# Optimization experiments

Measured on AMD Instinct MI355X. Metric: run time of the kernel, lower is better.

## Reference

```python
import jax, jax.numpy as jnp
import numpy as np

B, N, K = 4, 2048, 30
H = 128   # num_hidden == num_V_dim
E = 128   # num_E_dim
SCALE = 30.0
EPS = 1e-5


def _ln(x, g, b):
    m = jnp.mean(x, axis=-1, keepdims=True)
    v = jnp.mean(jnp.square(x - m), axis=-1, keepdims=True)
    return (x - m) * jax.lax.rsqrt(v + EPS) * g + b


def _gather_nodes(h_V, E_idx):
    # h_V: [B,N,D], E_idx: [B,N,K] -> [B,N,K,D]
    b, n, k = E_idx.shape
    flat = E_idx.reshape(b, n * k)
    g = jnp.take_along_axis(h_V, flat[:, :, None], axis=1)
    return g.reshape(b, n, k, h_V.shape[-1])


def _gelu(x):
    return jax.nn.gelu(x, approximate=False)  # torch GELU default (erf)


def _lin(x, w, b):
    return jnp.einsum('...i,oi->...o', x, w) + b


def setup_inputs() -> dict:
    key = jax.random.key(0)
    ks = jax.random.split(key, 24)
    s = 0.05
    inp = {
        'h_V': jax.random.normal(ks[0], (B, N, H), jnp.float32),
        'h_E': jax.random.normal(ks[1], (B, N, K, E), jnp.float32),
        'E_idx': jax.random.randint(ks[2], (B, N, K), 0, N, jnp.int32),
        'mask_V': jnp.ones((B, N), jnp.float32),
        'mask_attend': jnp.ones((B, N, K), jnp.float32),
        # node-update MLP W1,W2,W3
        'W1_w': jax.random.normal(ks[3], (H, E + 2 * H), jnp.float32) * s,
        'W1_b': jnp.zeros((H,), jnp.float32),
        'W2_w': jax.random.normal(ks[4], (H, H), jnp.float32) * s,
        'W2_b': jnp.zeros((H,), jnp.float32),
        'W3_w': jax.random.normal(ks[5], (H, H), jnp.float32) * s,
        'W3_b': jnp.zeros((H,), jnp.float32),
        # edge-update MLP W11,W12,W13
        'W11_w': jax.random.normal(ks[6], (H, E + 2 * H), jnp.float32) * s,
        'W11_b': jnp.zeros((H,), jnp.float32),
        'W12_w': jax.random.normal(ks[7], (H, H), jnp.float32) * s,
        'W12_b': jnp.zeros((H,), jnp.float32),
        'W13_w': jax.random.normal(ks[8], (E, H), jnp.float32) * s,
        'W13_b': jnp.zeros((E,), jnp.float32),
        # dense FFN
        'Win_w': jax.random.normal(ks[9], (4 * H, H), jnp.float32) * s,
        'Win_b': jnp.zeros((4 * H,), jnp.float32),
        'Wout_w': jax.random.normal(ks[10], (H, 4 * H), jnp.float32) * s,
        'Wout_b': jnp.zeros((H,), jnp.float32),
        # layer norms
        'g1': jnp.ones((H,), jnp.float32), 'b1': jnp.zeros((H,), jnp.float32),
        'g2': jnp.ones((H,), jnp.float32), 'b2': jnp.zeros((H,), jnp.float32),
        'g3': jnp.ones((E,), jnp.float32), 'b3': jnp.zeros((E,), jnp.float32),
    }
    return inp


def reference(h_V, h_E, E_idx, mask_V, mask_attend,
              W1_w, W1_b, W2_w, W2_b, W3_w, W3_b,
              W11_w, W11_b, W12_w, W12_b, W13_w, W13_b,
              Win_w, Win_b, Wout_w, Wout_b,
              g1, b1, g2, b2, g3, b3):
    # --- node update ---
    nb = _gather_nodes(h_V, E_idx)                               # [B,N,K,H]
    hV_exp = jnp.broadcast_to(h_V[:, :, None, :], nb.shape)
    h_EV = jnp.concatenate([hV_exp, h_E, nb], axis=-1)           # [B,N,K,E+2H]
    m = _lin(_gelu(_lin(_gelu(_lin(h_EV, W1_w, W1_b)), W2_w, W2_b)), W3_w, W3_b)
    m = mask_attend[..., None] * m
    dh = jnp.sum(m, axis=-2) / SCALE
    h_V = _ln(h_V + dh, g1, b1)
    dh = _lin(_gelu(_lin(h_V, Win_w, Win_b)), Wout_w, Wout_b)
    h_V = _ln(h_V + dh, g2, b2)
    h_V = mask_V[..., None] * h_V
    # --- edge update ---
    nb = _gather_nodes(h_V, E_idx)
    hV_exp = jnp.broadcast_to(h_V[:, :, None, :], nb.shape)
    h_EV = jnp.concatenate([hV_exp, h_E, nb], axis=-1)
    m = _lin(_gelu(_lin(_gelu(_lin(h_EV, W11_w, W11_b)), W12_w, W12_b)), W13_w, W13_b)
    h_E = _ln(h_E + m, g3, b3)
    return h_V, h_E
```

## Files before the change

kernel.cpp:

```cpp
#include <hip/hip_runtime.h>
#include <math.h>

#define Kn    30
#define Hn    128
#define NB    2048
#define YS    136

#define OFF_W1    0
#define OFF_W2    49152
#define OFF_W3    65536
#define OFF_W11   81920
#define OFF_W12   131072
#define OFF_W13   147456
#define OFF_WIN   163840
#define OFF_WOUT  229376
#define W_TOTAL   294912
#define WS_ZM     524288
#define WS_SS     1048576
#define WS_SN     2097152

typedef __attribute__((ext_vector_type(8)))  short bh8;
typedef __attribute__((ext_vector_type(4)))  short bh4;
typedef __attribute__((ext_vector_type(16))) float fx16;

__device__ __forceinline__ unsigned short f2bf(float f) {
    unsigned int u = __float_as_uint(f);
    u += 0x7fffu + ((u >> 16) & 1u);
    return (unsigned short)(u >> 16);
}
__device__ __forceinline__ float bf2f(unsigned short h) {
    return __uint_as_float(((unsigned int)h) << 16);
}
__device__ __forceinline__ float gelu_f(float x) {
    float x2 = x * x;
    float p  = fmaf(x2, -0.10294415f, -2.30218409f);
    float e  = exp2f(x * p);
    return x * __builtin_amdgcn_rcpf(1.0f + e);
}
__device__ __forceinline__ fx16 mfma_bf16(bh8 a, bh8 b, fx16 c) {
    return __builtin_amdgcn_mfma_f32_32x32x16_bf16(a, b, c, 0, 0, 0);
}
__device__ __forceinline__ void st_bf4(unsigned short* dst, float4 v) {
    bh4 t;
    t.x = (short)f2bf(v.x); t.y = (short)f2bf(v.y);
    t.z = (short)f2bf(v.z); t.w = (short)f2bf(v.w);
    *(bh4*)dst = t;
}

template<int KS>
__device__ __forceinline__ void gemm_one(const unsigned short* __restrict__ aBase,
                                         const unsigned short* __restrict__ b0,
                                         fx16& acc0) {
    #pragma unroll
    for (int ks = 0; ks < KS; ks++) {
        bh8 a = *(const bh8*)(aBase + ks * 16);
        acc0 = mfma_bf16(a, *(const bh8*)(b0 + ks * 16), acc0);
    }
}

__device__ __forceinline__ void epi1_gelu_sg(const fx16& ac, int col,
                                             float bias, const float* __restrict__ sSelf,
                                             const float* __restrict__ nbrCol,
                                             const int* __restrict__ sIdx,
                                             unsigned short* __restrict__ dst, int lane) {
    int ro = 4 * (lane >> 5);
    float st = sSelf[col] + bias;
    #pragma unroll
    for (int r = 0; r < 16; r++) {
        int row = ro + (r & 3) + 8 * (r >> 2);
        float pn = nbrCol[(size_t)sIdx[row] * Hn];
        dst[row * YS + col] = f2bf(gelu_f(ac[r] + st + pn));
    }
}
__device__ __forceinline__ void epi1_gelu(const fx16& ac, int col,
                                          float bias, unsigned short* __restrict__ dst,
                                          int lane) {
    int ro = 4 * (lane >> 5);
    #pragma unroll
    for (int r = 0; r < 16; r++) {
        int row = ro + (r & 3) + 8 * (r >> 2);
        dst[row * YS + col] = f2bf(gelu_f(ac[r] + bias));
    }
}
__device__ __forceinline__ void epi1_plain(const fx16& ac, int col,
                                           float bias, unsigned short* __restrict__ dst,
                                           int lane) {
    int ro = 4 * (lane >> 5);
    #pragma unroll
    for (int r = 0; r < 16; r++) {
        int row = ro + (r & 3) + 8 * (r >> 2);
        dst[row * YS + col] = f2bf(ac[r] + bias);
    }
}

__global__ __launch_bounds__(256) void prep_weights(
    const float* __restrict__ W1, const float* __restrict__ W2,
    const float* __restrict__ W3, const float* __restrict__ W11,
    const float* __restrict__ W12, const float* __restrict__ W13,
    const float* __restrict__ Win, const float* __restrict__ Wout,
    unsigned short* __restrict__ wsbf) {
    int i = blockIdx.x * 256 + threadIdx.x;
    if (i >= W_TOTAL) return;
    float v;
    if      (i < OFF_W2)   v = W1[i - OFF_W1];
    else if (i < OFF_W3)   v = W2[i - OFF_W2];
    else if (i < OFF_W11)  v = W3[i - OFF_W3];
    else if (i < OFF_W12)  v = W11[i - OFF_W11];
    else if (i < OFF_W13)  v = W12[i - OFF_W12];
    else if (i < OFF_WIN)  v = W13[i - OFF_W13];
    else if (i < OFF_WOUT) v = Win[i - OFF_WIN];
    else                   v = Wout[i - OFF_WOUT];
    wsbf[i] = f2bf(v);
}

__global__ __launch_bounds__(256) void self_gemm(
    const float* __restrict__ hv, const unsigned short* __restrict__ wsbf,
    float* __restrict__ s1s, float* __restrict__ s1n) {
    __shared__ __align__(16) unsigned short sA[32 * YS];
    const int tid = threadIdx.x;
    const int p0 = blockIdx.x * 32;
    const unsigned short* W1bf = wsbf + OFF_W1;
    for (int i = tid; i < 1024; i += 256) {
        int r = i >> 5, c4 = (i & 31) << 2;
        float4 v = *(const float4*)(hv + (size_t)(p0 + r) * Hn + c4);
        st_bf4(sA + r * YS + c4, v);
    }
    __syncthreads();
    const int wid = tid >> 6, lane = tid & 63;
    const int lane31 = lane & 31, lk = (lane >> 5) << 3;
    fx16 accS = {}, accN = {};
    const unsigned short* a   = sA + lane31 * YS + lk;
    const unsigned short* bwS = W1bf + (size_t)(32 * wid + lane31) * 384 + lk;
    const unsigned short* bwN = bwS + 256;
    #pragma unroll
    for (int ks = 0; ks < 8; ks++) {
        bh8 av = *(const bh8*)(a + ks * 16);
        accS = mfma_bf16(av, *(const bh8*)(bwS + ks * 16), accS);
        accN = mfma_bf16(av, *(const bh8*)(bwN + ks * 16), accN);
    }
    int col = 32 * wid + lane31;
    #pragma unroll
    for (int r = 0; r < 16; r++) {
        int row = (r & 3) + 8 * (r >> 2) + 4 * (lane >> 5);
        s1s[(size_t)(p0 + row) * Hn + col] = accS[r];
        s1n[(size_t)(p0 + row) * Hn + col] = accN[r];
    }
}

__global__ __launch_bounds__(256, 8) void node_msg_mfma(
    const float* __restrict__ h_E, const int* __restrict__ E_idx,
    const float* __restrict__ mask_attend,
    const unsigned short* __restrict__ wsbf,
    const float* __restrict__ s1s, const float* __restrict__ s1n,
    const float* __restrict__ W1_b, const float* __restrict__ W2_b,
    unsigned short* __restrict__ zbf, float* __restrict__ zm) {
    __shared__ __align__(16) unsigned short sX[32 * YS];
    __shared__ __align__(16) unsigned short sY[32 * YS];
    __shared__ float sS1[128];
    __shared__ float sMask[32];
    __shared__ int   sIdx[32];

    const int tid = threadIdx.x;
    const int p = blockIdx.x;
    const int bB = p >> 11;
    const unsigned short* W1bf = wsbf + OFF_W1;
    const unsigned short* W2bf = wsbf + OFF_W2;

    for (int i = tid; i < 960; i += 256) {
        int r = i >> 5, c4 = (i & 31) << 2;
        float4 v = *(const float4*)(h_E + ((size_t)p * Kn + r) * Hn + c4);
        st_bf4(sX + r * YS + c4, v);
    }
    if (tid < 136)
        ((unsigned int*)(sX + 30 * YS))[tid] = 0;
    if (tid < 32) {
        int c4 = tid << 2;
        *(float4*)(sS1 + c4) = *(const float4*)(s1s + (size_t)p * Hn + c4);
    }
    if (tid < 32) {
        sMask[tid] = (tid < Kn) ? mask_attend[p * Kn + tid] : 0.f;
        sIdx[tid]  = (tid < Kn) ? E_idx[p * Kn + tid] : 0;
    }
    __syncthreads();

    const int wid = tid >> 6, lane = tid & 63;
    const int lane31 = lane & 31, lk = (lane >> 5) << 3;
    const fx16 zv = {};
    const int col = 32 * wid + lane31;

    fx16 acc = zv;
    gemm_one<8>(sX + lane31 * YS + lk,
                W1bf + (size_t)col * 384 + 128 + lk, acc);
    epi1_gelu_sg(acc, col, W1_b[col], sS1,
                 s1n + (size_t)bB * NB * Hn + col, sIdx, sY, lane);
    __syncthreads();

    acc = zv;
    gemm_one<8>(sY + lane31 * YS + lk,
                W2bf + (size_t)col * 128 + lk, acc);
    {
        float bias = W2_b[col];
        float sum = 0.f;
        #pragma unroll
        for (int r = 0; r < 16; r++) {
            int row = (r & 3) + 8 * (r >> 2) + 4 * (lane >> 5);
            if (row < Kn) sum += gelu_f(acc[r] + bias) * sMask[row];
        }
        sum += __shfl_down(sum, 32);
        if (lane < 32)
            zbf[(size_t)p * Hn + col] = f2bf(sum * (1.0f / 30.0f));
    }
    if (tid == 0) {
        float s = 0.f;
        #pragma unroll
        for (int k = 0; k < Kn; k++) s += sMask[k];
        zm[p] = s * (1.0f / 30.0f);
    }
}

__global__ __launch_bounds__(256) void node_fin_ffn(
    const unsigned short* __restrict__ zbf, const float* __restrict__ zm,
    const float* __restrict__ h_V, const float* __restrict__ mask_V,
    const unsigned short* __restrict__ wsbf,
    const float* __restrict__ W3_b, const float* __restrict__ Win_b,
    const float* __restrict__ Wout_b,
    const float* __restrict__ g1v, const float* __restrict__ b1v,
    const float* __restrict__ g2v, const float* __restrict__ b2v,
    float* __restrict__ hV_out, float* __restrict__ s11s, float* __restrict__ s11n) {
    __shared__ __align__(16) unsigned short sA[32 * YS];
    __shared__ __align__(16) unsigned short sH[32 * YS];
    __shared__ __align__(16) float sO[32 * 132];
    __shared__ __align__(16) float sM[32 * 132];
    __shared__ __align__(16) unsigned short sV[32 * YS];
    __shared__ float sZm[32];

    const int tid = threadIdx.x;
    const int p0 = blockIdx.x * 32;
    const unsigned short* W3bf   = wsbf + OFF_W3;
    const unsigned short* Winbf  = wsbf + OFF_WIN;
    const unsigned short* Woutbf = wsbf + OFF_WOUT;
    const unsigned short* W11bf  = wsbf + OFF_W11;

    for (int i = tid; i < 512; i += 256) {
        int r = i >> 4, c8 = (i & 15) << 3;
        *(bh8*)(sA + r * YS + c8) = *(const bh8*)(zbf + (size_t)(p0 + r) * Hn + c8);
    }
    if (tid < 32) sZm[tid] = zm[p0 + tid];
    __syncthreads();

    const int wid = tid >> 6, lane = tid & 63;
    const int lane31 = lane & 31, lk = (lane >> 5) << 3;
    const fx16 zv = {};

    {
        fx16 acc = zv;
        const unsigned short* a  = sA + lane31 * YS + lk;
        const unsigned short* bw = W3bf + (size_t)(32 * wid + lane31) * 128 + lk;
        #pragma unroll
        for (int ks = 0; ks < 8; ks++)
            acc = mfma_bf16(*(const bh8*)(a + ks * 16), *(const bh8*)(bw + ks * 16), acc);
        int col = 32 * wid + lane31;
        float bias = W3_b[col];
        #pragma unroll
        for (int r = 0; r < 16; r++) {
            int row = (r & 3) + 8 * (r >> 2) + 4 * (lane >> 5);
            sO[row * 132 + col] = acc[r] + sZm[row] * bias;
        }
    }
    __syncthreads();

    for (int r = wid; r < 32; r += 4) {
        float x0 = sO[r * 132 + lane]      + h_V[(size_t)(p0 + r) * Hn + lane];
        float x1 = sO[r * 132 + 64 + lane] + h_V[(size_t)(p0 + r) * Hn + 64 + lane];
        float s = x0 + x1, q = x0 * x0 + x1 * x1;
        #pragma unroll
        for (int off = 32; off; off >>= 1) { s += __shfl_down(s, off); q += __shfl_down(q, off); }
        s = __shfl(s, 0); q = __shfl(q, 0);
        float mean = s * 0.0078125f;
        float rstd = rsqrtf(q * 0.0078125f - mean * mean + 1e-5f);
        float m0 = (x0 - mean) * rstd * g1v[lane]      + b1v[lane];
        float m1 = (x1 - mean) * rstd * g1v[lane + 64] + b1v[lane + 64];
        sM[r * 132 + lane]      = m0;
        sM[r * 132 + 64 + lane] = m1;
        sA[r * YS + lane]      = f2bf(m0);
        sA[r * YS + 64 + lane] = f2bf(m1);
    }
    __syncthreads();

    fx16 accO = zv;
    for (int c = 0; c < 4; c++) {
        int hcol = 128 * c + 32 * wid + lane31;
        fx16 t = zv;
        {
            const unsigned short* a  = sA + lane31 * YS + lk;
            const unsigned short* bw = Winbf + (size_t)hcol * 128 + lk;
            #pragma unroll
            for (int ks = 0; ks < 8; ks++)
                t = mfma_bf16(*(const bh8*)(a + ks * 16), *(const bh8*)(bw + ks * 16), t);
        }
        float bias = Win_b[hcol];
        int colL = 32 * wid + lane31;
        #pragma unroll
        for (int r = 0; r < 16; r++) {
            int row = (r & 3) + 8 * (r >> 2) + 4 * (lane >> 5);
            sH[row * YS + colL] = f2bf(gelu_f(t[r] + bias));
        }
        __syncthreads();
        {
            const unsigned short* a  = sH + lane31 * YS + lk;
            const unsigned short* bw = Woutbf + (size_t)(32 * wid + lane31) * 512 + 128 * c + lk;
            #pragma unroll
            for (int ks = 0; ks < 8; ks++)
                accO = mfma_bf16(*(const bh8*)(a + ks * 16), *(const bh8*)(bw + ks * 16), accO);
        }
        __syncthreads();
    }
    {
        int col = 32 * wid + lane31;
        float bias = Wout_b[col];
        #pragma unroll
        for (int r = 0; r < 16; r++) {
            int row = (r & 3) + 8 * (r >> 2) + 4 * (lane >> 5);
            sO[row * 132 + col] = accO[r] + bias;
        }
    }
    __syncthreads();

    for (int r = wid; r < 32; r += 4) {
        float x0 = sO[r * 132 + lane]      + sM[r * 132 + lane];
        float x1 = sO[r * 132 + 64 + lane] + sM[r * 132 + 64 + lane];
        float s = x0 + x1, q = x0 * x0 + x1 * x1;
        #pragma unroll
        for (int off = 32; off; off >>= 1) { s += __shfl_down(s, off); q += __shfl_down(q, off); }
        s = __shfl(s, 0); q = __shfl(q, 0);
        float mean = s * 0.0078125f;
        float rstd = rsqrtf(q * 0.0078125f - mean * mean + 1e-5f);
        float mv = mask_V[p0 + r];
        float y0 = ((x0 - mean) * rstd * g2v[lane]      + b2v[lane])      * mv;
        float y1 = ((x1 - mean) * rstd * g2v[lane + 64] + b2v[lane + 64]) * mv;
        hV_out[(size_t)(p0 + r) * Hn + lane]      = y0;
        hV_out[(size_t)(p0 + r) * Hn + 64 + lane] = y1;
        sV[r * YS + lane]      = f2bf(y0);
        sV[r * YS + 64 + lane] = f2bf(y1);
    }
    __syncthreads();

    {
        int col = 32 * wid + lane31;
        fx16 accS = zv, accN = zv;
        const unsigned short* a   = sV + lane31 * YS + lk;
        const unsigned short* bwS = W11bf + (size_t)col * 384 + lk;
        const unsigned short* bwN = W11bf + (size_t)col * 384 + 256 + lk;
        #pragma unroll
        for (int ks = 0; ks < 8; ks++) {
            bh8 av = *(const bh8*)(a + ks * 16);
            accS = mfma_bf16(av, *(const bh8*)(bwS + ks * 16), accS);
            accN = mfma_bf16(av, *(const bh8*)(bwN + ks * 16), accN);
        }
        #pragma unroll
        for (int r = 0; r < 16; r++) {
            int row = (r & 3) + 8 * (r >> 2) + 4 * (lane >> 5);
            s11s[(size_t)(p0 + row) * Hn + col] = accS[r];
            s11n[(size_t)(p0 + row) * Hn + col] = accN[r];
        }
    }
}

__global__ __launch_bounds__(256, 8) void edge_update_mfma(
    const float* __restrict__ h_E, const int* __restrict__ E_idx,
    const unsigned short* __restrict__ wsbf,
    const float* __restrict__ s11s, const float* __restrict__ s11n,
    const float* __restrict__ W11_b, const float* __restrict__ W12_b,
    const float* __restrict__ W13_b,
    const float* __restrict__ g3v, const float* __restrict__ b3v,
    float* __restrict__ hE_out) {
    __shared__ __align__(16) unsigned short sX[32 * YS];
    __shared__ __align__(16) unsigned short sY[32 * YS];
    __shared__ float sS11[128];
    __shared__ int   sIdx[32];

    const int tid = threadIdx.x;
    const int p = blockIdx.x;
    const int bB = p >> 11;
    const unsigned short* W11bf = wsbf + OFF_W11;
    const unsigned short* W12bf = wsbf + OFF_W12;
    const unsigned short* W13bf = wsbf + OFF_W13;

    for (int i = tid; i < 960; i += 256) {
        int r = i >> 5, c4 = (i & 31) << 2;
        float4 v = *(const float4*)(h_E + ((size_t)p * Kn + r) * Hn + c4);
        st_bf4(sX + r * YS + c4, v);
    }
    if (tid < 136)
        ((unsigned int*)(sX + 30 * YS))[tid] = 0;
    if (tid < 32) {
        int c4 = tid << 2;
        *(float4*)(sS11 + c4) = *(const float4*)(s11s + (size_t)p * Hn + c4);
    }
    if (tid < 32) sIdx[tid] = (tid < Kn) ? E_idx[p * Kn + tid] : 0;
    __syncthreads();

    const int wid = tid >> 6, lane = tid & 63;
    const int lane31 = lane & 31, lk = (lane >> 5) << 3;
    const fx16 zv = {};
    const int col = 32 * wid + lane31;

    fx16 acc = zv;
    gemm_one<8>(sX + lane31 * YS + lk,
                W11bf + (size_t)col * 384 + 128 + lk, acc);
    epi1_gelu_sg(acc, col, W11_b[col], sS11,
                 s11n + (size_t)bB * NB * Hn + col, sIdx, sY, lane);
    __syncthreads();

    acc = zv;
    gemm_one<8>(sY + lane31 * YS + lk,
                W12bf + (size_t)col * 128 + lk, acc);
    __syncthreads();
    epi1_gelu(acc, col, W12_b[col], sY, lane);
    __syncthreads();

    acc = zv;
    gemm_one<8>(sY + lane31 * YS + lk,
                W13bf + (size_t)col * 128 + lk, acc);
    __syncthreads();
    epi1_plain(acc, col, W13_b[col], sY, lane);
    __syncthreads();

    for (int r = wid; r < Kn; r += 4) {
        float x0 = bf2f(sX[r * YS + lane])      + bf2f(sY[r * YS + lane]);
        float x1 = bf2f(sX[r * YS + 64 + lane]) + bf2f(sY[r * YS + 64 + lane]);
        float s = x0 + x1, q = x0 * x0 + x1 * x1;
        #pragma unroll
        for (int off = 32; off; off >>= 1) { s += __shfl_down(s, off); q += __shfl_down(q, off); }
        s = __shfl(s, 0); q = __shfl(q, 0);
        float mean = s * 0.0078125f;
        float rstd = rsqrtf(q * 0.0078125f - mean * mean + 1e-5f);
        float* op = hE_out + ((size_t)p * Kn + r) * Hn;
        op[lane]      = (x0 - mean) * rstd * g3v[lane]      + b3v[lane];
        op[lane + 64] = (x1 - mean) * rstd * g3v[lane + 64] + b3v[lane + 64];
    }
}

extern "C" void kernel_launch(void* const* d_in, const int* in_sizes, int n_in,
                              void* d_out, int out_size, void* d_ws, size_t ws_size,
                              hipStream_t stream) {
    const float* h_V         = (const float*)d_in[0];
    const float* h_E         = (const float*)d_in[1];
    const int*   E_idx       = (const int*)  d_in[2];
    const float* mask_V      = (const float*)d_in[3];
    const float* mask_attend = (const float*)d_in[4];
    const float* W1_w  = (const float*)d_in[5];
    const float* W1_b  = (const float*)d_in[6];
    const float* W2_w  = (const float*)d_in[7];
    const float* W2_b  = (const float*)d_in[8];
    const float* W3_w  = (const float*)d_in[9];
    const float* W3_b  = (const float*)d_in[10];
    const float* W11_w = (const float*)d_in[11];
    const float* W11_b = (const float*)d_in[12];
    const float* W12_w = (const float*)d_in[13];
    const float* W12_b = (const float*)d_in[14];
    const float* W13_w = (const float*)d_in[15];
    const float* W13_b = (const float*)d_in[16];
    const float* Win_w  = (const float*)d_in[17];
    const float* Win_b  = (const float*)d_in[18];
    const float* Wout_w = (const float*)d_in[19];
    const float* Wout_b = (const float*)d_in[20];
    const float* g1 = (const float*)d_in[21];
    const float* b1 = (const float*)d_in[22];
    const float* g2 = (const float*)d_in[23];
    const float* b2 = (const float*)d_in[24];
    const float* g3 = (const float*)d_in[25];
    const float* b3 = (const float*)d_in[26];

    float* out    = (float*)d_out;
    float* hV_out = out;
    float* hE_out = out + (size_t)4 * 2048 * 128;
    unsigned short* wsbf = (unsigned short*)d_ws;
    float* wsf = (float*)(wsbf + W_TOTAL);
    unsigned short* zbf = (unsigned short*)wsf;
    float* zm = wsf + WS_ZM;
    float* sS = wsf + WS_SS;
    float* sN = wsf + WS_SN;

    prep_weights<<<(W_TOTAL + 255) / 256, 256, 0, stream>>>(
        W1_w, W2_w, W3_w, W11_w, W12_w, W13_w, Win_w, Wout_w, wsbf);

    self_gemm<<<256, 256, 0, stream>>>(h_V, wsbf, sS, sN);

    node_msg_mfma<<<8192, 256, 0, stream>>>(
        h_E, E_idx, mask_attend, wsbf, sS, sN, W1_b, W2_b, zbf, zm);

    node_fin_ffn<<<256, 256, 0, stream>>>(
        zbf, zm, h_V, mask_V, wsbf, W3_b, Win_b, Wout_b,
        g1, b1, g2, b2, hV_out, sS, sN);

    edge_update_mfma<<<8192, 256, 0, stream>>>(
        h_E, E_idx, wsbf, sS, sN,
        W11_b, W12_b, W13_b, g3, b3, hE_out);
}
```

Measured before the change: 473.1 us.

## Pre-convert h_E to padded bf16 tiles once and fuse prep kernels

A combined prep kernel converts the weights to bf16, computes the self-projection GEMM, and writes h_E as padded bf16 per-node tiles into workspace. The node-message and edge-update kernels then copy these tiles straight into LDS instead of each converting fp32 h_E. The goal is to remove the duplicated fp32 load and convert work and one kernel launch. In exchange it adds a bf16 tile write plus two tile reads, which can raise total memory traffic. The tiled path is used only if the workspace is large enough, with the old path as a fallback.

Result: slower. 500.1 us (+5.7%).

```diff
diff --git a/kernel.cpp b/kernel.cpp
--- a/kernel.cpp
+++ b/kernel.cpp
@@ -5,6 +5,7 @@
 #define Hn    128
 #define NB    2048
 #define YS    136
+#define TILE_SH 4608
 
 #define OFF_W1    0
 #define OFF_W2    49152
@@ -18,6 +19,7 @@
 #define WS_ZM     524288
 #define WS_SS     1048576
 #define WS_SN     2097152
+#define WS_TILE_F 3145728
 
 typedef __attribute__((ext_vector_type(8)))  short bh8;
 typedef __attribute__((ext_vector_type(4)))  short bh4;
@@ -45,6 +47,16 @@
     t.x = (short)f2bf(v.x); t.y = (short)f2bf(v.y);
     t.z = (short)f2bf(v.z); t.w = (short)f2bf(v.w);
     *(bh4*)dst = t;
+}
+__device__ __forceinline__ bh8 ld_bf8(const float* __restrict__ p) {
+    float4 a = *(const float4*)p;
+    float4 b = *(const float4*)(p + 4);
+    bh8 r;
+    r[0] = (short)f2bf(a.x); r[1] = (short)f2bf(a.y);
+    r[2] = (short)f2bf(a.z); r[3] = (short)f2bf(a.w);
+    r[4] = (short)f2bf(b.x); r[5] = (short)f2bf(b.y);
+    r[6] = (short)f2bf(b.z); r[7] = (short)f2bf(b.w);
+    return r;
 }
 
 template<int KS>
@@ -90,6 +102,76 @@
     for (int r = 0; r < 16; r++) {
         int row = ro + (r & 3) + 8 * (r >> 2);
         dst[row * YS + col] = f2bf(ac[r] + bias);
+    }
+}
+
+__global__ __launch_bounds__(256) void prep_all(
+    const float* __restrict__ h_E, const float* __restrict__ h_V,
+    const float* __restrict__ W1, const float* __restrict__ W2,
+    const float* __restrict__ W3, const float* __restrict__ W11,
+    const float* __restrict__ W12, const float* __restrict__ W13,
+    const float* __restrict__ Win, const float* __restrict__ Wout,
+    unsigned short* __restrict__ wsbf, unsigned short* __restrict__ hEt,
+    float* __restrict__ s1s, float* __restrict__ s1n) {
+    __shared__ __align__(16) unsigned short sA[32 * YS];
+    const int b = blockIdx.x;
+    const int tid = threadIdx.x;
+
+    if (b < 1152) {
+        int i = b * 256 + tid;
+        if (i < W_TOTAL) {
+            float v;
+            if      (i < OFF_W2)   v = W1[i - OFF_W1];
+            else if (i < OFF_W3)   v = W2[i - OFF_W2];
+            else if (i < OFF_W11)  v = W3[i - OFF_W3];
+            else if (i < OFF_W12)  v = W11[i - OFF_W11];
+            else if (i < OFF_W13)  v = W12[i - OFF_W12];
+            else if (i < OFF_WIN)  v = W13[i - OFF_W13];
+            else if (i < OFF_WOUT) v = Win[i - OFF_WIN];
+            else                   v = Wout[i - OFF_WOUT];
+            wsbf[i] = f2bf(v);
+        }
+        return;
+    }
+    if (b < 9344) {
+        int p = b - 1152;
+        unsigned short* tile = hEt + (size_t)p * TILE_SH;
+        for (int i = tid; i < 960; i += 256) {
+            int r = i >> 5, c4 = (i & 31) << 2;
+            float4 v = *(const float4*)(h_E + ((size_t)p * Kn + r) * Hn + c4);
+            st_bf4(tile + r * YS + c4, v);
+        }
+        for (int i = tid; i < 528; i += 256)
+            tile[4080 + i] = 0;
+        return;
+    }
+    {
+        const int p0 = (b - 9344) * 32;
+        for (int i = tid; i < 1024; i += 256) {
+            int r = i >> 5, c4 = (i & 31) << 2;
+            float4 v = *(const float4*)(h_V + (size_t)(p0 + r) * Hn + c4);
+            st_bf4(sA + r * YS + c4, v);
+        }
+        __syncthreads();
+        const int wid = tid >> 6, lane = tid & 63;
+        const int lane31 = lane & 31, lk = (lane >> 5) << 3;
+        fx16 accS = {}, accN = {};
+        const unsigned short* a = sA + lane31 * YS + lk;
+        const float* wrS = W1 + (size_t)(32 * wid + lane31) * 384 + lk;
+        const float* wrN = wrS + 256;
+        #pragma unroll
+        for (int ks = 0; ks < 8; ks++) {
+            bh8 av = *(const bh8*)(a + ks * 16);
+            accS = mfma_bf16(av, ld_bf8(wrS + ks * 16), accS);
+            accN = mfma_bf16(av, ld_bf8(wrN + ks * 16), accN);
+        }
+        int col = 32 * wid + lane31;
+        #pragma unroll
+        for (int r = 0; r < 16; r++) {
+            int row = (r & 3) + 8 * (r >> 2) + 4 * (lane >> 5);
+            s1s[(size_t)(p0 + row) * Hn + col] = accS[r];
+            s1n[(size_t)(p0 + row) * Hn + col] = accN[r];
+        }
     }
 }
 
@@ -147,14 +229,15 @@
     }
 }
 
+template<int TILED>
 __global__ __launch_bounds__(256, 8) void node_msg_mfma(
-    const float* __restrict__ h_E, const int* __restrict__ E_idx,
-    const float* __restrict__ mask_attend,
+    const float* __restrict__ h_E, const unsigned short* __restrict__ hEt,
+    const int* __restrict__ E_idx, const float* __restrict__ mask_attend,
     const unsigned short* __restrict__ wsbf,
     const float* __restrict__ s1s, const float* __restrict__ s1n,
     const float* __restrict__ W1_b, const float* __restrict__ W2_b,
     unsigned short* __restrict__ zbf, float* __restrict__ zm) {
-    __shared__ __align__(16) unsigned short sX[32 * YS];
+    __shared__ __align__(16) unsigned short sX[TILE_SH];
     __shared__ __align__(16) unsigned short sY[32 * YS];
     __shared__ float sS1[128];
     __shared__ float sMask[32];
@@ -166,13 +249,19 @@
     const unsigned short* W1bf = wsbf + OFF_W1;
     const unsigned short* W2bf = wsbf + OFF_W2;
 
-    for (int i = tid; i < 960; i += 256) {
-        int r = i >> 5, c4 = (i & 31) << 2;
-        float4 v = *(const float4*)(h_E + ((size_t)p * Kn + r) * Hn + c4);
-        st_bf4(sX + r * YS + c4, v);
-    }
-    if (tid < 136)
-        ((unsigned int*)(sX + 30 * YS))[tid] = 0;
+    if (TILED) {
+        const unsigned short* tile = hEt + (size_t)p * TILE_SH;
+        for (int i = tid; i < 576; i += 256)
+            *(bh8*)(sX + i * 8) = *(const bh8*)(tile + i * 8);
+    } else {
+        for (int i = tid; i < 960; i += 256) {
+            int r = i >> 5, c4 = (i & 31) << 2;
+            float4 v = *(const float4*)(h_E + ((size_t)p * Kn + r) * Hn + c4);
+            st_bf4(sX + r * YS + c4, v);
+        }
+        if (tid < 136)
+            ((unsigned int*)(sX + 30 * YS))[tid] = 0;
+    }
     if (tid < 32) {
         int c4 = tid << 2;
         *(float4*)(sS1 + c4) = *(const float4*)(s1s + (size_t)p * Hn + c4);
@@ -366,15 +455,17 @@
     }
 }
 
+template<int TILED>
 __global__ __launch_bounds__(256, 8) void edge_update_mfma(
-    const float* __restrict__ h_E, const int* __restrict__ E_idx,
+    const float* __restrict__ h_E, const unsigned short* __restrict__ hEt,
+    const int* __restrict__ E_idx,
     const unsigned short* __restrict__ wsbf,
     const float* __restrict__ s11s, const float* __restrict__ s11n,
     const float* __restrict__ W11_b, const float* __restrict__ W12_b,
     const float* __restrict__ W13_b,
     const float* __restrict__ g3v, const float* __restrict__ b3v,
     float* __restrict__ hE_out) {
-    __shared__ __align__(16) unsigned short sX[32 * YS];
+    __shared__ __align__(16) unsigned short sX[TILE_SH];
     __shared__ __align__(16) unsigned short sY[32 * YS];
     __shared__ float sS11[128];
     __shared__ int   sIdx[32];
@@ -386,13 +477,19 @@
     const unsigned short* W12bf = wsbf + OFF_W12;
     const unsigned short* W13bf = wsbf + OFF_W13;
 
-    for (int i = tid; i < 960; i += 256) {
-        int r = i >> 5, c4 = (i & 31) << 2;
-        float4 v = *(const float4*)(h_E + ((size_t)p * Kn + r) * Hn + c4);
-        st_bf4(sX + r * YS + c4, v);
-    }
-    if (tid < 136)
-        ((unsigned int*)(sX + 30 * YS))[tid] = 0;
+    if (TILED) {
+        const unsigned short* tile = hEt + (size_t)p * TILE_SH;
+        for (int i = tid; i < 576; i += 256)
+            *(bh8*)(sX + i * 8) = *(const bh8*)(tile + i * 8);
+    } else {
+        for (int i = tid; i < 960; i += 256) {
+            int r = i >> 5, c4 = (i & 31) << 2;
+            float4 v = *(const float4*)(h_E + ((size_t)p * Kn + r) * Hn + c4);
+            st_bf4(sX + r * YS + c4, v);
+        }
+        if (tid < 136)
+            ((unsigned int*)(sX + 30 * YS))[tid] = 0;
+    }
     if (tid < 32) {
         int c4 = tid << 2;
         *(float4*)(sS11 + c4) = *(const float4*)(s11s + (size_t)p * Hn + c4);
@@ -481,20 +578,35 @@
     float* zm = wsf + WS_ZM;
     float* sS = wsf + WS_SS;
     float* sN = wsf + WS_SN;
-
-    prep_weights<<<(W_TOTAL + 255) / 256, 256, 0, stream>>>(
-        W1_w, W2_w, W3_w, W11_w, W12_w, W13_w, Win_w, Wout_w, wsbf);
-
-    self_gemm<<<256, 256, 0, stream>>>(h_V, wsbf, sS, sN);
-
-    node_msg_mfma<<<8192, 256, 0, stream>>>(
-        h_E, E_idx, mask_attend, wsbf, sS, sN, W1_b, W2_b, zbf, zm);
-
-    node_fin_ffn<<<256, 256, 0, stream>>>(
-        zbf, zm, h_V, mask_V, wsbf, W3_b, Win_b, Wout_b,
-        g1, b1, g2, b2, hV_out, sS, sN);
-
-    edge_update_mfma<<<8192, 256, 0, stream>>>(
-        h_E, E_idx, wsbf, sS, sN,
-        W11_b, W12_b, W13_b, g3, b3, hE_out);
-}
+    unsigned short* hEt = (unsigned short*)(wsf + WS_TILE_F);
+
+    const size_t need = (size_t)W_TOTAL * 2 + (size_t)WS_TILE_F * 4
+                      + (size_t)8192 * TILE_SH * 2;
+    const bool tiled = (ws_size >= need);
+
+    if (tiled) {
+        prep_all<<<9600, 256, 0, stream>>>(
+            h_E, h_V, W1_w, W2_w, W3_w, W11_w, W12_w, W13_w, Win_w, Wout_w,
+            wsbf, hEt, sS, sN);
+        node_msg_mfma<1><<<8192, 256, 0, stream>>>(
+            h_E, hEt, E_idx, mask_attend, wsbf, sS, sN, W1_b, W2_b, zbf, zm);
+        node_fin_ffn<<<256, 256, 0, stream>>>(
+            zbf, zm, h_V, mask_V, wsbf, W3_b, Win_b, Wout_b,
+            g1, b1, g2, b2, hV_out, sS, sN);
+        edge_update_mfma<1><<<8192, 256, 0, stream>>>(
+            h_E, hEt, E_idx, wsbf, sS, sN,
+            W11_b, W12_b, W13_b, g3, b3, hE_out);
+    } else {
+        prep_weights<<<1152, 256, 0, stream>>>(
+            W1_w, W2_w, W3_w, W11_w, W12_w, W13_w, Win_w, Wout_w, wsbf);
+        self_gemm<<<256, 256, 0, stream>>>(h_V, wsbf, sS, sN);
+        node_msg_mfma<0><<<8192, 256, 0, stream>>>(
+            h_E, hEt, E_idx, mask_attend, wsbf, sS, sN, W1_b, W2_b, zbf, zm);
+        node_fin_ffn<<<256, 256, 0, stream>>>(
+            zbf, zm, h_V, mask_V, wsbf, W3_b, Win_b, Wout_b,
+            g1, b1, g2, b2, hV_out, sS, sN);
+        edge_update_mfma<0><<<8192, 256, 0, stream>>>(
+            h_E, hEt, E_idx, wsbf, sS, sN,
+            W11_b, W12_b, W13_b, g3, b3, hE_out);
+    }
+}
```
